# Optimization experiments

Measured on AMD Instinct MI355X. Metric: run time of the kernel, lower is better.

## Reference

```python
import jax, jax.numpy as jnp
import numpy as np

N_LM = 468
BS = 512
N = BS * N_LM          # 239616 nodes total
E = N * 16             # 3833856 edges
IN_C = 64
OUT_C = 128
K = 3
EPS = 1e-5


def _uniform(key, shape, fan_in):
    s = 1.0 / np.sqrt(fan_in)
    return jax.random.uniform(key, shape, jnp.float32, -s, s)


def setup_inputs() -> dict:
    key = jax.random.key(0)
    ks = jax.random.split(key, 10)
    x = jax.random.normal(ks[0], (N, IN_C), jnp.float32)
    edge_index = jax.random.randint(ks[1], (2, E), 0, N, dtype=jnp.int64)
    return {
        "x": x,
        "edge_index": edge_index,
        "num_landmarks": N_LM,
        # GraphConv params (PyG: lin_rel has bias, lin_root has no bias)
        "W_rel": _uniform(ks[2], (IN_C, OUT_C), IN_C),
        "b_rel": _uniform(ks[3], (OUT_C,), IN_C),
        "W_root": _uniform(ks[4], (IN_C, OUT_C), IN_C),
        # tcn: BN1 -> ReLU -> Conv1d(OUT_C,OUT_C,3,pad=1) -> BN2 -> ReLU
        "bn1_g": jnp.ones((OUT_C,), jnp.float32),
        "bn1_b": jnp.zeros((OUT_C,), jnp.float32),
        "conv_w": _uniform(ks[5], (OUT_C, OUT_C, K), OUT_C * K),
        "conv_b": _uniform(ks[6], (OUT_C,), OUT_C * K),
        "bn2_g": jnp.ones((OUT_C,), jnp.float32),
        "bn2_b": jnp.zeros((OUT_C,), jnp.float32),
        # residual Conv1d(IN_C, OUT_C, 1)
        "res_w": _uniform(ks[7], (OUT_C, IN_C, 1), IN_C),
        "res_b": _uniform(ks[8], (OUT_C,), IN_C),
    }


def _batchnorm_train(h, g, b):
    # h: [bs, C, L]; training-mode BN over (batch, length)
    mean = h.mean(axis=(0, 2), keepdims=True)
    var = ((h - mean) ** 2).mean(axis=(0, 2), keepdims=True)
    return (h - mean) * jax.lax.rsqrt(var + EPS) * g[None, :, None] + b[None, :, None]


def _conv1d(h, w, pad):
    # h: [bs, C_in, L], w: [C_out, C_in, K]
    return jax.lax.conv_general_dilated(
        h, w, window_strides=(1,), padding=((pad, pad),),
        dimension_numbers=("NCH", "OIH", "NCH"))


def reference(x, edge_index, num_landmarks, W_rel, b_rel, W_root,
              bn1_g, bn1_b, conv_w, conv_b, bn2_g, bn2_b, res_w, res_b):
    # GraphConv: sum-aggregate neighbor features, then two linear maps
    src, dst = edge_index[0], edge_index[1]
    agg = jax.ops.segment_sum(x[src], dst, num_segments=x.shape[0])  # [N, IN_C]
    h = agg @ W_rel + b_rel + x @ W_root                              # [N, OUT_C]

    bs = x.shape[0] // num_landmarks
    h = h.reshape(bs, num_landmarks, OUT_C).transpose(0, 2, 1)        # [bs, OUT_C, L]

    h = jax.nn.relu(_batchnorm_train(h, bn1_g, bn1_b))
    h = _conv1d(h, conv_w, pad=(K - 1) // 2) + conv_b[None, :, None]
    h = jax.nn.relu(_batchnorm_train(h, bn2_g, bn2_b))

    r = x.reshape(bs, num_landmarks, IN_C).transpose(0, 2, 1)         # [bs, IN_C, L]
    r = _conv1d(r, res_w, pad=0) + res_b[None, :, None]               # [bs, OUT_C, L]

    out = h + r
    out = out.transpose(0, 2, 1).reshape(-1, OUT_C)                   # [N, OUT_C]
    return out
```

## Files before the change

kernel.cpp:

```cpp
#include <hip/hip_runtime.h>

#define N_NODES 239616
#define NLM 468
#define BSZ 512
#define NEDGE 3833856
#define IN_C 64
#define OUT_C 128
#define KW 3
#define EPSV 1e-5f

#define GM 128
#define LCH 128
#define NCHK 4
#define NBUCK 117
#define BCH 4096
#define BCAP 36864
#define NSUM 8

typedef __attribute__((ext_vector_type(8))) __bf16 bf16x8;
typedef __attribute__((ext_vector_type(4))) float f32x4;

__device__ inline unsigned short f2bf(float f) {
    unsigned int u = __builtin_bit_cast(unsigned int, f);
    u = (u + 0x7FFFu + ((u >> 16) & 1u)) >> 16;
    return (unsigned short)u;
}
__device__ inline float bf2f(unsigned short b) {
    return __builtin_bit_cast(float, (unsigned)b << 16);
}


__global__ void k_binit(int* __restrict__ gbcnt) {
    int b = threadIdx.x;
    if (b < NBUCK) gbcnt[b] = b * BCAP;
}

__global__ __launch_bounds__(256) void k_bucket(const int* __restrict__ ei,
                                                int* __restrict__ gbcnt,
                                                unsigned* __restrict__ bp) {
    __shared__ int h[128], sc[128], cur2[128], base[128];
    __shared__ unsigned long long pairs[BCH];
    const int t = threadIdx.x;
    const int e0 = blockIdx.x * BCH;

    if (t < 128) h[t] = 0;
    __syncthreads();

    int d[16], s[16];
    #pragma unroll
    for (int i = 0; i < 16; ++i) {
        int e = e0 + i * 256 + t;
        d[i] = ei[NEDGE + e];
        s[i] = ei[e];
    }
    #pragma unroll
    for (int i = 0; i < 16; ++i) atomicAdd(&h[d[i] >> 11], 1);
    __syncthreads();

    if (t < 128) sc[t] = h[t];
    __syncthreads();
    for (int dd = 1; dd < 128; dd <<= 1) {
        int v = 0;
        if (t < 128 && t >= dd) v = sc[t - dd];
        __syncthreads();
        if (t < 128) sc[t] += v;
        __syncthreads();
    }
    if (t < 128) {
        int excl = sc[t] - h[t];
        cur2[t] = excl;
        base[t] = (h[t] > 0) ? atomicAdd(&gbcnt[t], h[t]) : 0;
    }
    __syncthreads();

    #pragma unroll
    for (int i = 0; i < 16; ++i) {
        int b = d[i] >> 11;
        int p = atomicAdd(&cur2[b], 1);
        pairs[p] = ((unsigned long long)(unsigned)d[i] << 32) | (unsigned)s[i];
    }
    __syncthreads();

    for (int i = t; i < BCH; i += 256) {
        unsigned long long pr = pairs[i];
        int dv = (int)(pr >> 32);
        int b = dv >> 11;
        int excl = sc[b] - h[b];
        bp[base[b] + (i - excl)] = ((unsigned)(dv & 2047) << 18) | (unsigned)(pr & 0x3ffffu);
    }
}

__global__ __launch_bounds__(1024) void k_fill3(const int* __restrict__ gbcnt,
                                                const unsigned* __restrict__ bp,
                                                int* __restrict__ hist,
                                                int* __restrict__ off,
                                                int* __restrict__ elist) {
    __shared__ int lh[2048];
    __shared__ int lcur[2048];
    __shared__ int ts[1024];
    const int b = blockIdx.x;
    const int lo = b * BCAP;
    const int hi = gbcnt[b];
    const int nbase = b * 2048;

    lh[threadIdx.x] = 0;
    lh[threadIdx.x + 1024] = 0;
    __syncthreads();

    for (int i = lo + threadIdx.x; i < hi; i += 1024) {
        atomicAdd(&lh[bp[i] >> 18], 1);
    }
    __syncthreads();

    int a0 = lh[2 * threadIdx.x];
    int a1 = lh[2 * threadIdx.x + 1];
    ts[threadIdx.x] = a0 + a1;
    __syncthreads();
    for (int d = 1; d < 1024; d <<= 1) {
        int v = (threadIdx.x >= d) ? ts[threadIdx.x - d] : 0;
        __syncthreads();
        ts[threadIdx.x] += v;
        __syncthreads();
    }
    int excl = ts[threadIdx.x] - (a0 + a1);
    int o0 = lo + excl;
    int o1 = o0 + a0;
    lcur[2 * threadIdx.x]     = o0;
    lcur[2 * threadIdx.x + 1] = o1;
    hist[nbase + 2 * threadIdx.x]     = a0;
    hist[nbase + 2 * threadIdx.x + 1] = a1;
    off[nbase + 2 * threadIdx.x]      = o0;
    off[nbase + 2 * threadIdx.x + 1]  = o1;
    __syncthreads();

    for (int i = lo + threadIdx.x; i < hi; i += 1024) {
        unsigned pr = bp[i];
        int pos = atomicAdd(&lcur[pr >> 18], 1);
        elist[pos] = (int)(pr & 0x3ffffu);
    }
}

__global__ __launch_bounds__(256) void k_xprep(const float* __restrict__ x,
                                               unsigned short* __restrict__ xb) {
    int i = blockIdx.x * 256 + threadIdx.x;
    float4 f0 = *reinterpret_cast<const float4*>(x + (size_t)i * 8);
    float4 f1 = *reinterpret_cast<const float4*>(x + (size_t)i * 8 + 4);
    uint4 u;
    u.x = f2bf(f0.x) | ((unsigned)f2bf(f0.y) << 16);
    u.y = f2bf(f0.z) | ((unsigned)f2bf(f0.w) << 16);
    u.z = f2bf(f1.x) | ((unsigned)f2bf(f1.y) << 16);
    u.w = f2bf(f1.z) | ((unsigned)f2bf(f1.w) << 16);
    *reinterpret_cast<uint4*>(xb + (size_t)i * 8) = u;
}

__global__ __launch_bounds__(256) void k_gather(const unsigned short* __restrict__ xb,
                                                const int* __restrict__ off,
                                                const int* __restrict__ hist,
                                                const int* __restrict__ elist,
                                                unsigned short* __restrict__ aggb) {
    int t = blockIdx.x * 256 + threadIdx.x;
    int n = t >> 3;
    int j = (t & 7) * 8;
    int start = off[n];
    int deg   = hist[n];
    float a[8];
    #pragma unroll
    for (int c = 0; c < 8; ++c) a[c] = 0.f;
    int i = 0;
    for (; i + 2 <= deg; i += 2) {
        int s0 = elist[start + i];
        int s1 = elist[start + i + 1];
        uint4 u0 = *reinterpret_cast<const uint4*>(xb + (size_t)s0 * IN_C + j);
        uint4 u1 = *reinterpret_cast<const uint4*>(xb + (size_t)s1 * IN_C + j);
        unsigned w0[4] = {u0.x, u0.y, u0.z, u0.w};
        unsigned w1[4] = {u1.x, u1.y, u1.z, u1.w};
        #pragma unroll
        for (int c = 0; c < 4; ++c) {
            a[2 * c]     += __builtin_bit_cast(float, w0[c] << 16);
            a[2 * c + 1] += __builtin_bit_cast(float, w0[c] & 0xffff0000u);
            a[2 * c]     += __builtin_bit_cast(float, w1[c] << 16);
            a[2 * c + 1] += __builtin_bit_cast(float, w1[c] & 0xffff0000u);
        }
    }
    if (i < deg) {
        int s0 = elist[start + i];
        uint4 u0 = *reinterpret_cast<const uint4*>(xb + (size_t)s0 * IN_C + j);
        unsigned w0[4] = {u0.x, u0.y, u0.z, u0.w};
        #pragma unroll
        for (int c = 0; c < 4; ++c) {
            a[2 * c]     += __builtin_bit_cast(float, w0[c] << 16);
            a[2 * c + 1] += __builtin_bit_cast(float, w0[c] & 0xffff0000u);
        }
    }
    uint4 o;
    o.x = f2bf(a[0]) | ((unsigned)f2bf(a[1]) << 16);
    o.y = f2bf(a[2]) | ((unsigned)f2bf(a[3]) << 16);
    o.z = f2bf(a[4]) | ((unsigned)f2bf(a[5]) << 16);
    o.w = f2bf(a[6]) | ((unsigned)f2bf(a[7]) << 16);
    *reinterpret_cast<uint4*>(aggb + (size_t)n * IN_C + j) = o;
}

__global__ __launch_bounds__(256) void k_wprep2(const float* __restrict__ Wrel,
                                                const float* __restrict__ Wroot,
                                                unsigned short* __restrict__ wG) {
    int i = blockIdx.x * 256 + threadIdx.x;
    int j    = i & 7;
    int lane = (i >> 3) & 63;
    int g    = (i >> 9) & 7;
    int ks   = i >> 12;
    int o    = g * 16 + (lane & 15);
    int k    = ks * 32 + ((lane >> 4) << 3) + j;
    float v = (k < IN_C) ? Wrel[k * OUT_C + o] : Wroot[(k - IN_C) * OUT_C + o];
    wG[i] = f2bf(v);
}

__global__ __launch_bounds__(256) void k_gemm1(const unsigned short* __restrict__ aggb,
                                               const unsigned short* __restrict__ xb,
                                               const unsigned short* __restrict__ wG,
                                               const float* __restrict__ brel,
                                               unsigned short* __restrict__ hb,
                                               float* __restrict__ sums) {
    __shared__ unsigned short tile[GM * 128];
    __shared__ float red[2][OUT_C];
    const int n0 = blockIdx.x * GM;

    for (int i = threadIdx.x; i < 2 * OUT_C; i += 256) (&red[0][0])[i] = 0.f;

    for (int i = threadIdx.x; i < GM * 16; i += 256) {
        int t = i >> 4, s = i & 15;
        const unsigned short* src = (s < 8) ? (aggb + (size_t)(n0 + t) * IN_C + s * 8)
                                            : (xb   + (size_t)(n0 + t) * IN_C + (s - 8) * 8);
        uint4 u = *reinterpret_cast<const uint4*>(src);
        int byte = t * 256 + (((s ^ (t & 7)) & 15) << 4);
        *reinterpret_cast<uint4*>(reinterpret_cast<char*>(tile) + byte) = u;
    }
    __syncthreads();

    const int w    = threadIdx.x >> 6;
    const int lane = threadIdx.x & 63;
    const int r16  = lane & 15;
    const int kg   = lane >> 4;

    f32x4 acc[2][8];
    #pragma unroll
    for (int rs = 0; rs < 2; ++rs)
        #pragma unroll
        for (int g = 0; g < 8; ++g)
            acc[rs][g] = (f32x4){0.f, 0.f, 0.f, 0.f};

    for (int ks = 0; ks < 4; ++ks) {
        bf16x8 a[2];
        #pragma unroll
        for (int rs = 0; rs < 2; ++rs) {
            const int t = w * 32 + rs * 16 + r16;
            const int slot = ks * 4 + kg;
            const int byte = t * 256 + (((slot ^ (t & 7)) & 15) << 4);
            uint4 u = *reinterpret_cast<const uint4*>(reinterpret_cast<const char*>(tile) + byte);
            a[rs] = __builtin_bit_cast(bf16x8, u);
        }
        #pragma unroll
        for (int g = 0; g < 8; ++g) {
            uint4 u = *reinterpret_cast<const uint4*>(wG + (((ks * 8 + g) * 64 + lane) << 3));
            bf16x8 b = __builtin_bit_cast(bf16x8, u);
            acc[0][g] = __builtin_amdgcn_mfma_f32_16x16x32_bf16(a[0], b, acc[0][g], 0, 0, 0);
            acc[1][g] = __builtin_amdgcn_mfma_f32_16x16x32_bf16(a[1], b, acc[1][g], 0, 0, 0);
        }
    }

    #pragma unroll
    for (int g = 0; g < 8; ++g) {
        const int col = g * 16 + r16;
        const float bias = brel[col];
        float s = 0.f, q = 0.f;
        #pragma unroll
        for (int rs = 0; rs < 2; ++rs) {
            #pragma unroll
            for (int reg = 0; reg < 4; ++reg) {
                const int row = n0 + w * 32 + rs * 16 + kg * 4 + reg;
                float v = acc[rs][g][reg] + bias;
                hb[(size_t)row * OUT_C + col] = f2bf(v);
                s += v;
                q += v * v;
            }
        }
        atomicAdd(&red[0][col], s);
        atomicAdd(&red[1][col], q);
    }
    __syncthreads();
    if (threadIdx.x < OUT_C) {
        float* sb = sums + (blockIdx.x & (NSUM - 1)) * 256;
        atomicAdd(&sb[threadIdx.x], red[0][threadIdx.x]);
        atomicAdd(&sb[128 + threadIdx.x], red[1][threadIdx.x]);
    }
}

__global__ void k_bnparams(const float* __restrict__ sums,
                           const float* __restrict__ g,
                           const float* __restrict__ b,
                           float* __restrict__ sc, float* __restrict__ sh) {
    int c = threadIdx.x;
    float s = 0.f, q = 0.f;
    #pragma unroll
    for (int r = 0; r < NSUM; ++r) {
        s += sums[r * 256 + c];
        q += sums[r * 256 + 128 + c];
    }
    const float inv_n = 1.0f / (float)N_NODES;
    float mean = s * inv_n;
    float var  = q * inv_n - mean * mean;
    float sv = g[c] * rsqrtf(var + EPSV);
    sc[c] = sv;
    sh[c] = b[c] - mean * sv;
}

__global__ __launch_bounds__(256) void k_wprep(const float* __restrict__ w,
                                               unsigned short* __restrict__ wBf) {
    int i = blockIdx.x * 256 + threadIdx.x;
    int j    = i & 7;
    int lane = (i >> 3) & 63;
    int g    = (i >> 9) & 7;
    int ks   = i >> 12;
    int o    = g * 16 + (lane & 15);
    int ci   = (ks & 3) * 32 + ((lane >> 4) << 3) + j;
    int ktap = ks >> 2;
    wBf[i] = f2bf(w[o * (OUT_C * KW) + ci * KW + ktap]);
}

__global__ __launch_bounds__(256) void k_wprep3(const float* __restrict__ rw,
                                                unsigned short* __restrict__ wR) {
    int i = blockIdx.x * 256 + threadIdx.x;
    int j    = i & 7;
    int lane = (i >> 3) & 63;
    int g    = (i >> 9) & 7;
    int ks   = i >> 12;
    int o    = g * 16 + (lane & 15);
    int k    = ks * 32 + ((lane >> 4) << 3) + j;
    wR[i] = f2bf(rw[o * IN_C + k]);
}

__global__ __launch_bounds__(256) void k_conv(const unsigned short* __restrict__ hb,
                                              const unsigned short* __restrict__ wBf,
                                              const float* __restrict__ cbv,
                                              const float* __restrict__ sc,
                                              const float* __restrict__ sh,
                                              unsigned short* __restrict__ cbuf,
                                              float* __restrict__ sums) {
    __shared__ unsigned short tile[(LCH + 2) * OUT_C];
    __shared__ float red[2][OUT_C];
    const int b  = blockIdx.x >> 2;
    const int ch = blockIdx.x & 3;
    const int l0 = ch * LCH;
    const unsigned short* hbp = hb + (size_t)b * NLM * OUT_C;

    for (int i = threadIdx.x; i < 2 * OUT_C; i += 256) (&red[0][0])[i] = 0.f;

    for (int i = threadIdx.x; i < (LCH + 2) * 16; i += 256) {
        int t = i >> 4;
        int s = i & 15;
        int l = l0 - 1 + t;
        uint4 u = make_uint4(0u, 0u, 0u, 0u);
        if (l >= 0 && l < NLM) {
            uint4 r = *reinterpret_cast<const uint4*>(hbp + (size_t)l * OUT_C + s * 8);
            unsigned wd[4] = {r.x, r.y, r.z, r.w};
            unsigned od[4];
            #pragma unroll
            for (int c2 = 0; c2 < 4; ++c2) {
                int c = s * 8 + c2 * 2;
                float lo = __builtin_bit_cast(float, wd[c2] << 16);
                float hi = __builtin_bit_cast(float, wd[c2] & 0xffff0000u);
                lo = fmaxf(0.f, lo * sc[c] + sh[c]);
                hi = fmaxf(0.f, hi * sc[c + 1] + sh[c + 1]);
                od[c2] = f2bf(lo) | ((unsigned)f2bf(hi) << 16);
            }
            u = make_uint4(od[0], od[1], od[2], od[3]);
        }
        int byte = t * 256 + (((s ^ (t & 7)) & 15) << 4);
        *reinterpret_cast<uint4*>(reinterpret_cast<char*>(tile) + byte) = u;
    }
    __syncthreads();

    const int w    = threadIdx.x >> 6;
    const int lane = threadIdx.x & 63;
    const int r16  = lane & 15;
    const int kg   = lane >> 4;

    f32x4 acc[8][2];
    #pragma unroll
    for (int rs = 0; rs < 8; ++rs)
        #pragma unroll
        for (int cs = 0; cs < 2; ++cs)
            acc[rs][cs] = (f32x4){0.f, 0.f, 0.f, 0.f};

    uint4 ucur0 = *reinterpret_cast<const uint4*>(wBf + (((0 * 8 + w * 2 + 0) * 64 + lane) << 3));
    uint4 ucur1 = *reinterpret_cast<const uint4*>(wBf + (((0 * 8 + w * 2 + 1) * 64 + lane) << 3));
    for (int ks = 0; ks < 12; ++ks) {
        uint4 unx0, unx1;
        if (ks < 11) {
            unx0 = *reinterpret_cast<const uint4*>(wBf + ((((ks + 1) * 8 + w * 2 + 0) * 64 + lane) << 3));
            unx1 = *reinterpret_cast<const uint4*>(wBf + ((((ks + 1) * 8 + w * 2 + 1) * 64 + lane) << 3));
        }
        bf16x8 b0 = __builtin_bit_cast(bf16x8, ucur0);
        bf16x8 b1 = __builtin_bit_cast(bf16x8, ucur1);
        const int ktap = ks >> 2;
        const int slotbase = (ks & 3) * 4 + kg;
        #pragma unroll
        for (int rs = 0; rs < 8; ++rs) {
            const int t = rs * 16 + r16 + ktap;
            const int byte = t * 256 + (((slotbase ^ (t & 7)) & 15) << 4);
            uint4 u = *reinterpret_cast<const uint4*>(reinterpret_cast<const char*>(tile) + byte);
            bf16x8 af = __builtin_bit_cast(bf16x8, u);
            acc[rs][0] = __builtin_amdgcn_mfma_f32_16x16x32_bf16(af, b0, acc[rs][0], 0, 0, 0);
            acc[rs][1] = __builtin_amdgcn_mfma_f32_16x16x32_bf16(af, b1, acc[rs][1], 0, 0, 0);
        }
        ucur0 = unx0;
        ucur1 = unx1;
    }

    #pragma unroll
    for (int cs = 0; cs < 2; ++cs) {
        const int col = w * 32 + cs * 16 + r16;
        const float bias = cbv[col];
        float s = 0.f, q = 0.f;
        #pragma unroll
        for (int rs = 0; rs < 8; ++rs) {
            #pragma unroll
            for (int reg = 0; reg < 4; ++reg) {
                int l = l0 + rs * 16 + kg * 4 + reg;
                if (l < NLM) {
                    float v = acc[rs][cs][reg] + bias;
                    cbuf[((size_t)b * NLM + l) * OUT_C + col] = f2bf(v);
                    s += v;
                    q += v * v;
                }
            }
        }
        atomicAdd(&red[0][col], s);
        atomicAdd(&red[1][col], q);
    }
    __syncthreads();
    if (threadIdx.x < OUT_C) {
        float* sb = sums + (blockIdx.x & (NSUM - 1)) * 256;
        atomicAdd(&sb[threadIdx.x], red[0][threadIdx.x]);
        atomicAdd(&sb[128 + threadIdx.x], red[1][threadIdx.x]);
    }
}

__global__ __launch_bounds__(256) void k_final(const unsigned short* __restrict__ cbuf,
                                               const unsigned short* __restrict__ xb,
                                               const unsigned short* __restrict__ wR,
                                               const float* __restrict__ rb,
                                               const float* __restrict__ sc,
                                               const float* __restrict__ sh,
                                               float* __restrict__ out) {
    __shared__ unsigned short tile[GM * IN_C];
    const int n0 = blockIdx.x * GM;

    for (int i = threadIdx.x; i < GM * 8; i += 256) {
        int t = i >> 3, s = i & 7;
        uint4 u = *reinterpret_cast<const uint4*>(xb + (size_t)(n0 + t) * IN_C + s * 8);
        int byte = t * 128 + (((s ^ (t & 7)) & 7) << 4);
        *reinterpret_cast<uint4*>(reinterpret_cast<char*>(tile) + byte) = u;
    }
    __syncthreads();

    const int w    = threadIdx.x >> 6;
    const int lane = threadIdx.x & 63;
    const int r16  = lane & 15;
    const int kg   = lane >> 4;

    f32x4 acc[2][8];
    #pragma unroll
    for (int rs = 0; rs < 2; ++rs)
        #pragma unroll
        for (int g = 0; g < 8; ++g)
            acc[rs][g] = (f32x4){0.f, 0.f, 0.f, 0.f};

    #pragma unroll
    for (int ks = 0; ks < 2; ++ks) {
        bf16x8 a[2];
        #pragma unroll
        for (int rs = 0; rs < 2; ++rs) {
            const int t = w * 32 + rs * 16 + r16;
            const int slot = ks * 4 + kg;
            const int byte = t * 128 + (((slot ^ (t & 7)) & 7) << 4);
            uint4 u = *reinterpret_cast<const uint4*>(reinterpret_cast<const char*>(tile) + byte);
            a[rs] = __builtin_bit_cast(bf16x8, u);
        }
        #pragma unroll
        for (int g = 0; g < 8; ++g) {
            uint4 u = *reinterpret_cast<const uint4*>(wR + (((ks * 8 + g) * 64 + lane) << 3));
            bf16x8 b = __builtin_bit_cast(bf16x8, u);
            acc[0][g] = __builtin_amdgcn_mfma_f32_16x16x32_bf16(a[0], b, acc[0][g], 0, 0, 0);
            acc[1][g] = __builtin_amdgcn_mfma_f32_16x16x32_bf16(a[1], b, acc[1][g], 0, 0, 0);
        }
    }

    #pragma unroll
    for (int g = 0; g < 8; ++g) {
        const int col = g * 16 + r16;
        const float bias = rb[col];
        const float scv = sc[col];
        const float shv = sh[col];
        #pragma unroll
        for (int rs = 0; rs < 2; ++rs) {
            #pragma unroll
            for (int reg = 0; reg < 4; ++reg) {
                const size_t row = (size_t)(n0 + w * 32 + rs * 16 + kg * 4 + reg);
                float cv = bf2f(cbuf[row * OUT_C + col]);
                out[row * OUT_C + col] = fmaxf(0.f, cv * scv + shv) + acc[rs][g][reg] + bias;
            }
        }
    }
}

extern "C" void kernel_launch(void* const* d_in, const int* in_sizes, int n_in,
                              void* d_out, int out_size, void* d_ws, size_t ws_size,
                              hipStream_t stream) {
    const float* x     = (const float*)d_in[0];
    const int*   ei    = (const int*)d_in[1];
    const float* Wrel  = (const float*)d_in[3];
    const float* brel  = (const float*)d_in[4];
    const float* Wroot = (const float*)d_in[5];
    const float* bn1g  = (const float*)d_in[6];
    const float* bn1b  = (const float*)d_in[7];
    const float* convw = (const float*)d_in[8];
    const float* convb = (const float*)d_in[9];
    const float* bn2g  = (const float*)d_in[10];
    const float* bn2b  = (const float*)d_in[11];
    const float* resw  = (const float*)d_in[12];
    const float* resb  = (const float*)d_in[13];
    float* out = (float*)d_out;

    unsigned short* aggb = (unsigned short*)d_ws;
    unsigned short* xb   = aggb + (size_t)N_NODES * IN_C;
    unsigned short* hb   = xb + (size_t)N_NODES * IN_C;
    unsigned short* cbuf = hb + (size_t)N_NODES * OUT_C;
    float* st = (float*)(cbuf + (size_t)N_NODES * OUT_C);
    float* sums1 = st;
    float* sums2 = st + 2048;
    float* sc1 = st + 4096; float* sh1 = st + 4224;
    float* sc2 = st + 4352; float* sh2 = st + 4480;
    unsigned short* wBf = (unsigned short*)(st + 4608);
    unsigned short* wG  = wBf + 49152;
    unsigned short* wR  = wG + 16384;

    int* hist   = (int*)hb;
    int* off    = hist + N_NODES;
    int* gbcnt  = off + N_NODES;
    int* elist  = gbcnt + 128;
    unsigned* bp = (unsigned*)(elist + NBUCK * BCAP);

    hipMemsetAsync(st, 0, 4096 * sizeof(float), stream);

    k_xprep <<<N_NODES / 32, 256, 0, stream>>>(x, xb);
    k_wprep <<<192, 256, 0, stream>>>(convw, wBf);
    k_wprep2<<<64, 256, 0, stream>>>(Wrel, Wroot, wG);
    k_wprep3<<<32, 256, 0, stream>>>(resw, wR);
    k_binit <<<1, 128, 0, stream>>>(gbcnt);
    k_bucket<<<NEDGE / BCH, 256, 0, stream>>>(ei, gbcnt, bp);
    k_fill3 <<<NBUCK, 1024, 0, stream>>>(gbcnt, bp, hist, off, elist);
    k_gather<<<(N_NODES * 8) / 256, 256, 0, stream>>>(xb, off, hist, elist, aggb);

    k_gemm1<<<N_NODES / GM, 256, 0, stream>>>(aggb, xb, wG, brel, hb, sums1);
    k_bnparams<<<1, 128, 0, stream>>>(sums1, bn1g, bn1b, sc1, sh1);
    k_conv<<<BSZ * NCHK, 256, 0, stream>>>(hb, wBf, convb, sc1, sh1, cbuf, sums2);
    k_bnparams<<<1, 128, 0, stream>>>(sums2, bn2g, bn2b, sc2, sh2);
    k_final<<<N_NODES / GM, 256, 0, stream>>>(cbuf, xb, wR, resb, sc2, sh2, out);
}
```

Baseline: 364.0 us.

## Fuse neighbor gather into GraphConv GEMM and stage output through LDS

Merges the gather kernel into the first GEMM: each block computes neighbor sums for its 128 nodes directly into the shared-memory A tile, so the aggregated bf16 buffer is never written to or read back from global memory. The GEMM epilogue now writes results into the LDS tile and then stores them to global as coalesced 16-byte rows instead of scattered 2-byte stores. The CSR scratch space moves from the hb buffer to cbuf because hb is now written while hist, off and elist are still being read. The trade-off is that the gather runs with only 1877 blocks of 256 threads, which gives less latency hiding for the random loads, and an extra barrier is added.

```diff
diff --git a/kernel.cpp b/kernel.cpp
--- a/kernel.cpp
+++ b/kernel.cpp
@@ -153,53 +153,6 @@
     *reinterpret_cast<uint4*>(xb + (size_t)i * 8) = u;
 }
 
-__global__ __launch_bounds__(256) void k_gather(const unsigned short* __restrict__ xb,
-                                                const int* __restrict__ off,
-                                                const int* __restrict__ hist,
-                                                const int* __restrict__ elist,
-                                                unsigned short* __restrict__ aggb) {
-    int t = blockIdx.x * 256 + threadIdx.x;
-    int n = t >> 3;
-    int j = (t & 7) * 8;
-    int start = off[n];
-    int deg   = hist[n];
-    float a[8];
-    #pragma unroll
-    for (int c = 0; c < 8; ++c) a[c] = 0.f;
-    int i = 0;
-    for (; i + 2 <= deg; i += 2) {
-        int s0 = elist[start + i];
-        int s1 = elist[start + i + 1];
-        uint4 u0 = *reinterpret_cast<const uint4*>(xb + (size_t)s0 * IN_C + j);
-        uint4 u1 = *reinterpret_cast<const uint4*>(xb + (size_t)s1 * IN_C + j);
-        unsigned w0[4] = {u0.x, u0.y, u0.z, u0.w};
-        unsigned w1[4] = {u1.x, u1.y, u1.z, u1.w};
-        #pragma unroll
-        for (int c = 0; c < 4; ++c) {
-            a[2 * c]     += __builtin_bit_cast(float, w0[c] << 16);
-            a[2 * c + 1] += __builtin_bit_cast(float, w0[c] & 0xffff0000u);
-            a[2 * c]     += __builtin_bit_cast(float, w1[c] << 16);
-            a[2 * c + 1] += __builtin_bit_cast(float, w1[c] & 0xffff0000u);
-        }
-    }
-    if (i < deg) {
-        int s0 = elist[start + i];
-        uint4 u0 = *reinterpret_cast<const uint4*>(xb + (size_t)s0 * IN_C + j);
-        unsigned w0[4] = {u0.x, u0.y, u0.z, u0.w};
-        #pragma unroll
-        for (int c = 0; c < 4; ++c) {
-            a[2 * c]     += __builtin_bit_cast(float, w0[c] << 16);
-            a[2 * c + 1] += __builtin_bit_cast(float, w0[c] & 0xffff0000u);
-        }
-    }
-    uint4 o;
-    o.x = f2bf(a[0]) | ((unsigned)f2bf(a[1]) << 16);
-    o.y = f2bf(a[2]) | ((unsigned)f2bf(a[3]) << 16);
-    o.z = f2bf(a[4]) | ((unsigned)f2bf(a[5]) << 16);
-    o.w = f2bf(a[6]) | ((unsigned)f2bf(a[7]) << 16);
-    *reinterpret_cast<uint4*>(aggb + (size_t)n * IN_C + j) = o;
-}
-
 __global__ __launch_bounds__(256) void k_wprep2(const float* __restrict__ Wrel,
                                                 const float* __restrict__ Wroot,
                                                 unsigned short* __restrict__ wG) {
@@ -214,25 +167,70 @@
     wG[i] = f2bf(v);
 }
 
-__global__ __launch_bounds__(256) void k_gemm1(const unsigned short* __restrict__ aggb,
-                                               const unsigned short* __restrict__ xb,
-                                               const unsigned short* __restrict__ wG,
-                                               const float* __restrict__ brel,
-                                               unsigned short* __restrict__ hb,
-                                               float* __restrict__ sums) {
+__global__ __launch_bounds__(256) void k_gg(const unsigned short* __restrict__ xb,
+                                            const int* __restrict__ off,
+                                            const int* __restrict__ hist,
+                                            const int* __restrict__ elist,
+                                            const unsigned short* __restrict__ wG,
+                                            const float* __restrict__ brel,
+                                            unsigned short* __restrict__ hb,
+                                            float* __restrict__ sums) {
     __shared__ unsigned short tile[GM * 128];
     __shared__ float red[2][OUT_C];
     const int n0 = blockIdx.x * GM;
 
     for (int i = threadIdx.x; i < 2 * OUT_C; i += 256) (&red[0][0])[i] = 0.f;
 
-    for (int i = threadIdx.x; i < GM * 16; i += 256) {
-        int t = i >> 4, s = i & 15;
-        const unsigned short* src = (s < 8) ? (aggb + (size_t)(n0 + t) * IN_C + s * 8)
-                                            : (xb   + (size_t)(n0 + t) * IN_C + (s - 8) * 8);
-        uint4 u = *reinterpret_cast<const uint4*>(src);
+    for (int i = threadIdx.x; i < GM * 8; i += 256) {
+        int t = i >> 3, s = 8 + (i & 7);
+        uint4 u = *reinterpret_cast<const uint4*>(xb + (size_t)(n0 + t) * IN_C + (i & 7) * 8);
         int byte = t * 256 + (((s ^ (t & 7)) & 15) << 4);
         *reinterpret_cast<uint4*>(reinterpret_cast<char*>(tile) + byte) = u;
+    }
+
+    for (int pass = 0; pass < 4; ++pass) {
+        const int tl = pass * 32 + (threadIdx.x >> 3);
+        const int n  = n0 + tl;
+        const int j  = (threadIdx.x & 7) * 8;
+        const int start = off[n];
+        const int deg   = hist[n];
+        float a[8];
+        #pragma unroll
+        for (int c = 0; c < 8; ++c) a[c] = 0.f;
+        int i = 0;
+        for (; i + 2 <= deg; i += 2) {
+            int s0 = elist[start + i];
+            int s1 = elist[start + i + 1];
+            uint4 u0 = *reinterpret_cast<const uint4*>(xb + (size_t)s0 * IN_C + j);
+            uint4 u1 = *reinterpret_cast<const uint4*>(xb + (size_t)s1 * IN_C + j);
+            unsigned w0[4] = {u0.x, u0.y, u0.z, u0.w};
+            unsigned w1[4] = {u1.x, u1.y, u1.z, u1.w};
+            #pragma unroll
+            for (int c = 0; c < 4; ++c) {
+                a[2 * c]     += __builtin_bit_cast(float, w0[c] << 16);
+                a[2 * c + 1] += __builtin_bit_cast(float, w0[c] & 0xffff0000u);
+                a[2 * c]     += __builtin_bit_cast(float, w1[c] << 16);
+                a[2 * c + 1] += __builtin_bit_cast(float, w1[c] & 0xffff0000u);
+            }
+        }
+        if (i < deg) {
+            int s0 = elist[start + i];
+            uint4 u0 = *reinterpret_cast<const uint4*>(xb + (size_t)s0 * IN_C + j);
+            unsigned w0[4] = {u0.x, u0.y, u0.z, u0.w};
+            #pragma unroll
+            for (int c = 0; c < 4; ++c) {
+                a[2 * c]     += __builtin_bit_cast(float, w0[c] << 16);
+                a[2 * c + 1] += __builtin_bit_cast(float, w0[c] & 0xffff0000u);
+            }
+        }
+        uint4 o;
+        o.x = f2bf(a[0]) | ((unsigned)f2bf(a[1]) << 16);
+        o.y = f2bf(a[2]) | ((unsigned)f2bf(a[3]) << 16);
+        o.z = f2bf(a[4]) | ((unsigned)f2bf(a[5]) << 16);
+        o.w = f2bf(a[6]) | ((unsigned)f2bf(a[7]) << 16);
+        const int s = j >> 3;
+        int byte = tl * 256 + (((s ^ (tl & 7)) & 15) << 4);
+        *reinterpret_cast<uint4*>(reinterpret_cast<char*>(tile) + byte) = o;
     }
     __syncthreads();
 
@@ -266,27 +264,37 @@
             acc[1][g] = __builtin_amdgcn_mfma_f32_16x16x32_bf16(a[1], b, acc[1][g], 0, 0, 0);
         }
     }
+    __syncthreads();
 
     #pragma unroll
     for (int g = 0; g < 8; ++g) {
-        const int col = g * 16 + r16;
+        const int col  = g * 16 + r16;
+        const int slot = col >> 3;
         const float bias = brel[col];
         float s = 0.f, q = 0.f;
         #pragma unroll
         for (int rs = 0; rs < 2; ++rs) {
             #pragma unroll
             for (int reg = 0; reg < 4; ++reg) {
-                const int row = n0 + w * 32 + rs * 16 + kg * 4 + reg;
+                const int rl = w * 32 + rs * 16 + kg * 4 + reg;
                 float v = acc[rs][g][reg] + bias;
-                hb[(size_t)row * OUT_C + col] = f2bf(v);
                 s += v;
                 q += v * v;
+                int byte = rl * 256 + (((slot ^ (rl & 7)) & 15) << 4) + (col & 7) * 2;
+                *reinterpret_cast<unsigned short*>(reinterpret_cast<char*>(tile) + byte) = f2bf(v);
             }
         }
         atomicAdd(&red[0][col], s);
         atomicAdd(&red[1][col], q);
     }
     __syncthreads();
+
+    for (int i = threadIdx.x; i < GM * 16; i += 256) {
+        int t = i >> 4, u = i & 15;
+        int byte = t * 256 + (((u ^ (t & 7)) & 15) << 4);
+        uint4 v = *reinterpret_cast<const uint4*>(reinterpret_cast<const char*>(tile) + byte);
+        *reinterpret_cast<uint4*>(hb + (size_t)(n0 + t) * OUT_C + u * 8) = v;
+    }
     if (threadIdx.x < OUT_C) {
         float* sb = sums + (blockIdx.x & (NSUM - 1)) * 256;
         atomicAdd(&sb[threadIdx.x], red[0][threadIdx.x]);
@@ -531,8 +539,7 @@
     const float* resb  = (const float*)d_in[13];
     float* out = (float*)d_out;
 
-    unsigned short* aggb = (unsigned short*)d_ws;
-    unsigned short* xb   = aggb + (size_t)N_NODES * IN_C;
+    unsigned short* xb   = (unsigned short*)d_ws;
     unsigned short* hb   = xb + (size_t)N_NODES * IN_C;
     unsigned short* cbuf = hb + (size_t)N_NODES * OUT_C;
     float* st = (float*)(cbuf + (size_t)N_NODES * OUT_C);
@@ -544,7 +551,7 @@
     unsigned short* wG  = wBf + 49152;
     unsigned short* wR  = wG + 16384;
 
-    int* hist   = (int*)hb;
+    int* hist   = (int*)cbuf;
     int* off    = hist + N_NODES;
     int* gbcnt  = off + N_NODES;
     int* elist  = gbcnt + 128;
@@ -559,9 +566,8 @@
     k_binit <<<1, 128, 0, stream>>>(gbcnt);
     k_bucket<<<NEDGE / BCH, 256, 0, stream>>>(ei, gbcnt, bp);
     k_fill3 <<<NBUCK, 1024, 0, stream>>>(gbcnt, bp, hist, off, elist);
-    k_gather<<<(N_NODES * 8) / 256, 256, 0, stream>>>(xb, off, hist, elist, aggb);
-
-    k_gemm1<<<N_NODES / GM, 256, 0, stream>>>(aggb, xb, wG, brel, hb, sums1);
+
+    k_gg<<<N_NODES / GM, 256, 0, stream>>>(xb, off, hist, elist, wG, brel, hb, sums1);
     k_bnparams<<<1, 128, 0, stream>>>(sums1, bn1g, bn1b, sc1, sh1);
     k_conv<<<BSZ * NCHK, 256, 0, stream>>>(hb, wBf, convb, sc1, sh1, cbuf, sums2);
     k_bnparams<<<1, 128, 0, stream>>>(sums2, bn2g, bn2b, sc2, sh2);
```

Result: slower. 383.1 us (+5.2%).

## Stage gemm1 output through LDS for coalesced stores and use 512 threads

Applied to the files above, without the earlier changes.

The first GEMM kernel now runs 512 threads per block, so each wave computes 16 rows instead of 32, which halves accumulator register use. The bf16 results are written into the swizzled shared tile and then copied to global memory as 16-byte row-contiguous stores, replacing scattered 2-byte stores. This is meant to cut global write transactions and raise occupancy. It adds an extra barrier and an LDS round-trip, and each wave now reuses the weight loads across fewer rows.

```diff
diff --git a/kernel.cpp b/kernel.cpp
--- a/kernel.cpp
+++ b/kernel.cpp
@@ -214,7 +214,7 @@
     wG[i] = f2bf(v);
 }
 
-__global__ __launch_bounds__(256) void k_gemm1(const unsigned short* __restrict__ aggb,
+__global__ __launch_bounds__(512) void k_gemm1(const unsigned short* __restrict__ aggb,
                                                const unsigned short* __restrict__ xb,
                                                const unsigned short* __restrict__ wG,
                                                const float* __restrict__ brel,
@@ -224,9 +224,9 @@
     __shared__ float red[2][OUT_C];
     const int n0 = blockIdx.x * GM;
 
-    for (int i = threadIdx.x; i < 2 * OUT_C; i += 256) (&red[0][0])[i] = 0.f;
-
-    for (int i = threadIdx.x; i < GM * 16; i += 256) {
+    for (int i = threadIdx.x; i < 2 * OUT_C; i += 512) (&red[0][0])[i] = 0.f;
+
+    for (int i = threadIdx.x; i < GM * 16; i += 512) {
         int t = i >> 4, s = i & 15;
         const unsigned short* src = (s < 8) ? (aggb + (size_t)(n0 + t) * IN_C + s * 8)
                                             : (xb   + (size_t)(n0 + t) * IN_C + (s - 8) * 8);
@@ -241,52 +241,51 @@
     const int r16  = lane & 15;
     const int kg   = lane >> 4;
 
-    f32x4 acc[2][8];
-    #pragma unroll
-    for (int rs = 0; rs < 2; ++rs)
-        #pragma unroll
-        for (int g = 0; g < 8; ++g)
-            acc[rs][g] = (f32x4){0.f, 0.f, 0.f, 0.f};
+    f32x4 acc[8];
+    #pragma unroll
+    for (int g = 0; g < 8; ++g) acc[g] = (f32x4){0.f, 0.f, 0.f, 0.f};
 
     for (int ks = 0; ks < 4; ++ks) {
-        bf16x8 a[2];
-        #pragma unroll
-        for (int rs = 0; rs < 2; ++rs) {
-            const int t = w * 32 + rs * 16 + r16;
-            const int slot = ks * 4 + kg;
-            const int byte = t * 256 + (((slot ^ (t & 7)) & 15) << 4);
-            uint4 u = *reinterpret_cast<const uint4*>(reinterpret_cast<const char*>(tile) + byte);
-            a[rs] = __builtin_bit_cast(bf16x8, u);
-        }
+        const int t = w * 16 + r16;
+        const int slot = ks * 4 + kg;
+        const int byte = t * 256 + (((slot ^ (t & 7)) & 15) << 4);
+        uint4 ua = *reinterpret_cast<const uint4*>(reinterpret_cast<const char*>(tile) + byte);
+        bf16x8 a = __builtin_bit_cast(bf16x8, ua);
         #pragma unroll
         for (int g = 0; g < 8; ++g) {
             uint4 u = *reinterpret_cast<const uint4*>(wG + (((ks * 8 + g) * 64 + lane) << 3));
             bf16x8 b = __builtin_bit_cast(bf16x8, u);
-            acc[0][g] = __builtin_amdgcn_mfma_f32_16x16x32_bf16(a[0], b, acc[0][g], 0, 0, 0);
-            acc[1][g] = __builtin_amdgcn_mfma_f32_16x16x32_bf16(a[1], b, acc[1][g], 0, 0, 0);
-        }
-    }
+            acc[g] = __builtin_amdgcn_mfma_f32_16x16x32_bf16(a, b, acc[g], 0, 0, 0);
+        }
+    }
+    __syncthreads();
 
     #pragma unroll
     for (int g = 0; g < 8; ++g) {
-        const int col = g * 16 + r16;
+        const int col  = g * 16 + r16;
+        const int slot = col >> 3;
         const float bias = brel[col];
         float s = 0.f, q = 0.f;
         #pragma unroll
-        for (int rs = 0; rs < 2; ++rs) {
-            #pragma unroll
-            for (int reg = 0; reg < 4; ++reg) {
-                const int row = n0 + w * 32 + rs * 16 + kg * 4 + reg;
-                float v = acc[rs][g][reg] + bias;
-                hb[(size_t)row * OUT_C + col] = f2bf(v);
-                s += v;
-                q += v * v;
-            }
+        for (int reg = 0; reg < 4; ++reg) {
+            const int rl = w * 16 + kg * 4 + reg;
+            float v = acc[g][reg] + bias;
+            s += v;
+            q += v * v;
+            int byte = rl * 256 + (((slot ^ (rl & 7)) & 15) << 4) + (col & 7) * 2;
+            *reinterpret_cast<unsigned short*>(reinterpret_cast<char*>(tile) + byte) = f2bf(v);
         }
         atomicAdd(&red[0][col], s);
         atomicAdd(&red[1][col], q);
     }
     __syncthreads();
+
+    for (int i = threadIdx.x; i < GM * 16; i += 512) {
+        int t = i >> 4, u = i & 15;
+        int byte = t * 256 + (((u ^ (t & 7)) & 15) << 4);
+        uint4 v = *reinterpret_cast<const uint4*>(reinterpret_cast<const char*>(tile) + byte);
+        *reinterpret_cast<uint4*>(hb + (size_t)(n0 + t) * OUT_C + u * 8) = v;
+    }
     if (threadIdx.x < OUT_C) {
         float* sb = sums + (blockIdx.x & (NSUM - 1)) * 256;
         atomicAdd(&sb[threadIdx.x], red[0][threadIdx.x]);
@@ -561,7 +560,7 @@
     k_fill3 <<<NBUCK, 1024, 0, stream>>>(gbcnt, bp, hist, off, elist);
     k_gather<<<(N_NODES * 8) / 256, 256, 0, stream>>>(xb, off, hist, elist, aggb);
 
-    k_gemm1<<<N_NODES / GM, 256, 0, stream>>>(aggb, xb, wG, brel, hb, sums1);
+    k_gemm1<<<N_NODES / GM, 512, 0, stream>>>(aggb, xb, wG, brel, hb, sums1);
     k_bnparams<<<1, 128, 0, stream>>>(sums1, bn1g, bn1b, sc1, sh1);
     k_conv<<<BSZ * NCHK, 256, 0, stream>>>(hb, wBf, convb, sc1, sh1, cbuf, sums2);
     k_bnparams<<<1, 128, 0, stream>>>(sums2, bn2g, bn2b, sc2, sh2);
```

Result: slower. 392.8 us (+7.9%).
